# Optimization experiments

Measured on AMD Instinct MI355X. Metric: run time of the kernel, lower is better.

## Reference

```python
import jax, jax.numpy as jnp
import numpy as np

L = 96
K = 3  # conv kernel size

def setup_inputs() -> dict:
    key = jax.random.key(0)
    ks = jax.random.split(key, 6)
    linear_x = jax.random.randint(ks[0], (4 * L**3,), 0, 2, dtype=jnp.int32)
    tetraeder_2 = jax.random.normal(ks[1], (2, 2), dtype=jnp.float32)
    w1 = jax.random.normal(ks[2], (K, K, K, 12, 16), dtype=jnp.float32) * 0.05
    b1 = jnp.zeros((16,), dtype=jnp.float32)
    w2 = jax.random.normal(ks[3], (K, K, K, 16, 32), dtype=jnp.float32) * 0.05
    b2 = jnp.zeros((32,), dtype=jnp.float32)
    wd = jax.random.normal(ks[4], (32, 1), dtype=jnp.float32) * 0.1
    return {"linear_x": linear_x, "tetraeder_2": tetraeder_2,
            "w1": w1, "b1": b1, "w2": w2, "b2": b2, "wd": wd}

def _bonds(linear_x, tetraeder_2):
    # x: (L,L,L,4) spin config; v: (L,L,L,4,d) per-site vectors via gather
    x = linear_x.reshape(L, L, L, 4)
    v = tetraeder_2[x]
    v0, v1, v2, v3 = v[..., 0, :], v[..., 1, :], v[..., 2, :], v[..., 3, :]
    # roll(v, 1, ax)[a] == v[(a-1) % L] -> periodic neighbor cells cell_1/2/3
    r1 = jnp.roll(v1, 1, axis=0)
    r2 = jnp.roll(v2, 1, axis=1)
    r3 = jnp.roll(v3, 1, axis=2)
    dot = lambda a, b: jnp.einsum('...d,...d->...', a, b)
    # 12 bonds in the exact order of on_unit_cell
    bonds = [dot(v0, v1), dot(v0, v2), dot(v0, v3),
             dot(v0, r1), dot(v0, r2), dot(v0, r3),
             dot(v1, v2), dot(v2, v3), dot(v3, v1),
             dot(r1, r2), dot(r2, r3), dot(r3, r1)]
    return jnp.stack(bonds, axis=-1)  # (L,L,L,12)

def _conv_block(y, w, b):
    pad = [(0, 0)] + [((K - 1) // 2, K // 2)] * 3 + [(0, 0)]
    y = jnp.pad(y, pad, mode='wrap')
    y = jax.lax.conv_general_dilated(
        y, w, window_strides=(1, 1, 1), padding='VALID',
        dimension_numbers=('NDHWC', 'DHWIO', 'NDHWC'))
    return jax.nn.elu(y + b)

def reference(linear_x, tetraeder_2, w1, b1, w2, b2, wd):
    y = _bonds(linear_x, tetraeder_2)[jnp.newaxis, ...]  # (1,L,L,L,12)
    y = _conv_block(y, w1, b1)
    y = _conv_block(y, w2, b2)
    y = jnp.mean(y, axis=(1, 2, 3)).ravel()  # (32,)
    return (y @ wd).ravel()[0]
```

## Files before the change

### kernel.cpp

```cpp
#include <hip/hip_runtime.h>
#include <hip/hip_bf16.h>
#include <cmath>

#define L 96
#define L3 (L*L*L)
#define NT 4
#define NCONV 864
#define BSTRIDE 456

__device__ __constant__ const int TAU[27] = {
    0,16,32, 288,304,320, 576,592,608,
    1728,1744,1760, 2016,2032,2048, 2304,2320,2336,
    3456,3472,3488, 3744,3760,3776, 4032,4048,4064};

typedef __attribute__((ext_vector_type(8))) short short8;
typedef __attribute__((ext_vector_type(4))) float floatx4;

__device__ __forceinline__ float eluf(float x) {
    float e = __expf(x) - 1.0f;
    return x > 0.0f ? x : e;
}

__device__ __forceinline__ unsigned short f2bf(float f) {
    __hip_bfloat16 h = __float2bfloat16(f);
    return *reinterpret_cast<unsigned short*>(&h);
}

__device__ __forceinline__ int wrapc(int x) {
    if (x < 0) x += L;
    if (x >= L) x -= L;
    return x;
}

__global__ __launch_bounds__(256) void prep_kernel(
    const int* __restrict__ lx, const float* __restrict__ tet,
    const float* __restrict__ w1, const float* __restrict__ w2,
    unsigned short* __restrict__ bnd,
    unsigned short* __restrict__ Bm1, unsigned short* __restrict__ Bm2)
{
    int idx = blockIdx.x * 256 + threadIdx.x;

    if (idx < 16*BSTRIDE) {
        int o = idx / BSTRIDE, k = idx % BSTRIDE;
        int tau = k >> 4, i = k & 15;
        float v = (k < 448 && tau < 27 && i < 12) ? w1[tau*192 + i*16 + o] : 0.0f;
        Bm1[idx] = f2bf(v);
    }
    int j = idx - 16*BSTRIDE;
    if (j >= 0 && j < 32*BSTRIDE) {
        int o = j / BSTRIDE, k = j % BSTRIDE;
        int tau = k >> 4;
        int i = k & 15;
        float v = (k < 448 && tau < 27) ? w2[tau*512 + i*32 + o] : 0.0f;
        Bm2[j] = f2bf(v);
    }

    int w = idx % L;
    int t = idx / L;
    int h = t % L;
    int d = t / L;

    float t00 = tet[0], t01 = tet[1], t10 = tet[2], t11 = tet[3];
    float d00 = t00*t00 + t01*t01;
    float d01 = t00*t10 + t01*t11;
    float d11 = t10*t10 + t11*t11;

    const int4 sv = *reinterpret_cast<const int4*>(lx + 4*idx);
    int s0 = sv.x, s1 = sv.y, s2 = sv.z, s3 = sv.w;
    int dm = (d == 0) ? L-1 : d-1;
    int hm = (h == 0) ? L-1 : h-1;
    int wm = (w == 0) ? L-1 : w-1;
    int r1 = lx[4*((dm*L + h)*L + w) + 1];
    int r2 = lx[4*((d*L + hm)*L + w) + 2];
    int r3 = lx[4*((d*L + h)*L + wm) + 3];

    auto dot = [&](int a, int b) -> float {
        return (a == b) ? (a ? d11 : d00) : d01;
    };

    union { unsigned short s[16]; int4 q[2]; } u;
    u.s[0]  = f2bf(dot(s0, s1));
    u.s[1]  = f2bf(dot(s0, s2));
    u.s[2]  = f2bf(dot(s0, s3));
    u.s[3]  = f2bf(dot(s0, r1));
    u.s[4]  = f2bf(dot(s0, r2));
    u.s[5]  = f2bf(dot(s0, r3));
    u.s[6]  = f2bf(dot(s1, s2));
    u.s[7]  = f2bf(dot(s2, s3));
    u.s[8]  = f2bf(dot(s3, s1));
    u.s[9]  = f2bf(dot(r1, r2));
    u.s[10] = f2bf(dot(r2, r3));
    u.s[11] = f2bf(dot(r3, r1));
    u.s[12] = 0; u.s[13] = 0; u.s[14] = 0; u.s[15] = 0;

    int4* dst = reinterpret_cast<int4*>(bnd + (size_t)idx*16);
    dst[0] = u.q[0];
    dst[1] = u.q[1];
}

__device__ __forceinline__ void stage_tile(
    const unsigned short* __restrict__ x, unsigned short* __restrict__ tile,
    int W0, int H0, int D0, int tid)
{
    #pragma unroll
    for (int i = 0; i < 6; ++i) {
        int t = tid + i*256;
        if (i < 5 || t < 1296) {
            int row = t / 36, off = t - row*36;
            int dd = row / 6, hh = row - dd*6;
            int gd = wrapc(D0 + dd - 1);
            int gh = wrapc(H0 + hh - 1);
            int vox = off >> 1, half = off & 1;
            int gw = wrapc(W0 + vox - 1);
            size_t gi = ((size_t)((gd*L + gh)*L + gw))*16 + half*8;
            __builtin_amdgcn_global_load_lds(
                (const __attribute__((address_space(1))) unsigned int*)(x + gi),
                (__attribute__((address_space(3))) unsigned int*)(tile + t*8),
                16, 0, 0);
        }
    }
}

__device__ __forceinline__ void stage_bmat(
    const unsigned short* __restrict__ Bm, unsigned short* __restrict__ Bls,
    int nxfer, int tid)
{
    #pragma unroll
    for (int i = 0; i < 8; ++i) {
        int t = tid + i*256;
        if (t < nxfer) {
            __builtin_amdgcn_global_load_lds(
                (const __attribute__((address_space(1))) unsigned int*)(Bm + t*8),
                (__attribute__((address_space(3))) unsigned int*)(Bls + t*8),
                16, 0, 0);
        }
    }
}

__device__ __forceinline__ void tile_coords(int& bid, int& W0, int& H0, int& Dz)
{
    bid = (blockIdx.z * 24 + blockIdx.y) * 6 + blockIdx.x;
    int nb = (bid & 7) * 108 + (bid >> 3);
    W0 = (nb % 6) * 16;
    int t1 = nb / 6;
    H0 = (t1 % 24) * 4;
    Dz = t1 / 24;
}

__global__ __launch_bounds__(256, 2) void conv1_kernel(
    const unsigned short* __restrict__ x, const unsigned short* __restrict__ Bm,
    const float* __restrict__ bias, unsigned short* __restrict__ y)
{
    __shared__ __attribute__((aligned(16))) unsigned short tile[2][6*6*18*16];
    __shared__ __attribute__((aligned(16))) unsigned short Bls[16*BSTRIDE];
    int tid = threadIdx.x;
    int bid, W0, H0, Dz;
    tile_coords(bid, W0, H0, Dz);

    stage_bmat(Bm, Bls, 912, tid);
    stage_tile(x, tile[0], W0, H0, Dz*16, tid);
    __syncthreads();

    int lane = tid & 63, wave = tid >> 6;
    int laneV = lane & 15, g = lane >> 4;
    int gb = g >> 1;
    int abase = laneV*16 + (g & 1)*8;
    float bch = bias[laneV];

    int moff[4];
    #pragma unroll
    for (int m = 0; m < 4; ++m) {
        int mt = wave*4 + m;
        moff[m] = (((mt >> 2)*6 + (mt & 3))*18)*16;
    }

    for (int t = 0; t < NT; ++t) {
        if (t < NT-1)
            stage_tile(x, tile[(t+1) & 1], W0, H0, Dz*16 + 4*(t+1), tid);

        const unsigned short* tl = tile[t & 1];

        floatx4 acc[4];
        #pragma unroll
        for (int m = 0; m < 4; ++m) acc[m] = (floatx4)(0.0f);

        short8 aC[4], aN[4], bC, bN;
        {
            int a0 = abase + (gb ? TAU[1] : TAU[0]);
            bC = *reinterpret_cast<const short8*>(&Bls[laneV*BSTRIDE + g*8]);
            #pragma unroll
            for (int m = 0; m < 4; ++m)
                aC[m] = *reinterpret_cast<const short8*>(&tl[moff[m] + a0]);
        }

        #pragma unroll
        for (int kt = 0; kt < 14; ++kt) {
            if (kt < 13) {
                int tev = TAU[2*(kt+1)];
                int tod = TAU[(2*(kt+1)+1 > 26) ? 26 : 2*(kt+1)+1];
                int an = abase + (gb ? tod : tev);
                bN = *reinterpret_cast<const short8*>(&Bls[laneV*BSTRIDE + (kt+1)*32 + g*8]);
                #pragma unroll
                for (int m = 0; m < 4; ++m)
                    aN[m] = *reinterpret_cast<const short8*>(&tl[moff[m] + an]);
            }
            __builtin_amdgcn_s_setprio(1);
            #pragma unroll
            for (int m = 0; m < 4; ++m)
                acc[m] = __builtin_amdgcn_mfma_f32_16x16x32_bf16(aC[m], bC, acc[m], 0, 0, 0);
            __builtin_amdgcn_s_setprio(0);
            if (kt < 13) {
                #pragma unroll
                for (int m = 0; m < 4; ++m) aC[m] = aN[m];
                bC = bN;
            }
        }

        int D0 = Dz*16 + t*4;
        #pragma unroll
        for (int m = 0; m < 4; ++m) {
            int mt = wave*4 + m;
            int d = D0 + (mt >> 2), h = H0 + (mt & 3);
            int wb = W0 + g*4;
            size_t base = ((size_t)((d*L + h)*L + wb))*16 + laneV;
            #pragma unroll
            for (int reg = 0; reg < 4; ++reg) {
                y[base + (size_t)reg*16] = f2bf(eluf(acc[m][reg] + bch));
            }
        }
        __syncthreads();
    }
}

__global__ __launch_bounds__(256, 2) void conv2_kernel(
    const unsigned short* __restrict__ x, const unsigned short* __restrict__ Bm,
    const float* __restrict__ bias, const float* __restrict__ wd,
    float* __restrict__ partials)
{
    __shared__ __attribute__((aligned(16))) unsigned short tile[2][6*6*18*16];
    __shared__ __attribute__((aligned(16))) unsigned short Bls[32*BSTRIDE];
    __shared__ float red[4];
    int tid = threadIdx.x;
    int bid, W0, H0, Dz;
    tile_coords(bid, W0, H0, Dz);

    stage_bmat(Bm, Bls, 1824, tid);
    stage_tile(x, tile[0], W0, H0, Dz*16, tid);
    __syncthreads();

    int lane = tid & 63, wave = tid >> 6;
    int laneV = lane & 15, g = lane >> 4;
    int gb = g >> 1;
    int abase = laneV*16 + (g & 1)*8;
    float b2a = bias[laneV], b2b = bias[16 + laneV];
    float wda = wd[laneV],  wdb = wd[16 + laneV];

    int moff[4];
    #pragma unroll
    for (int m = 0; m < 4; ++m) {
        int mt = wave*4 + m;
        moff[m] = (((mt >> 2)*6 + (mt & 3))*18)*16;
    }

    float s = 0.0f;

    for (int t = 0; t < NT; ++t) {
        if (t < NT-1)
            stage_tile(x, tile[(t+1) & 1], W0, H0, Dz*16 + 4*(t+1), tid);

        const unsigned short* tl = tile[t & 1];

        floatx4 acc[4][2];
        #pragma unroll
        for (int m = 0; m < 4; ++m) {
            acc[m][0] = (floatx4)(0.0f);
            acc[m][1] = (floatx4)(0.0f);
        }

        short8 aC[4], aN[4], bC0, bC1, bN0, bN1;
        {
            int a0 = abase + (gb ? TAU[1] : TAU[0]);
            bC0 = *reinterpret_cast<const short8*>(&Bls[laneV*BSTRIDE + g*8]);
            bC1 = *reinterpret_cast<const short8*>(&Bls[(16 + laneV)*BSTRIDE + g*8]);
            #pragma unroll
            for (int m = 0; m < 4; ++m)
                aC[m] = *reinterpret_cast<const short8*>(&tl[moff[m] + a0]);
        }

        #pragma unroll
        for (int kt = 0; kt < 14; ++kt) {
            if (kt < 13) {
                int tev = TAU[2*(kt+1)];
                int tod = TAU[(2*(kt+1)+1 > 26) ? 26 : 2*(kt+1)+1];
                int an = abase + (gb ? tod : tev);
                bN0 = *reinterpret_cast<const short8*>(&Bls[laneV*BSTRIDE + (kt+1)*32 + g*8]);
                bN1 = *reinterpret_cast<const short8*>(&Bls[(16 + laneV)*BSTRIDE + (kt+1)*32 + g*8]);
                #pragma unroll
                for (int m = 0; m < 4; ++m)
                    aN[m] = *reinterpret_cast<const short8*>(&tl[moff[m] + an]);
            }
            __builtin_amdgcn_s_setprio(1);
            #pragma unroll
            for (int m = 0; m < 4; ++m) {
                acc[m][0] = __builtin_amdgcn_mfma_f32_16x16x32_bf16(aC[m], bC0, acc[m][0], 0, 0, 0);
                acc[m][1] = __builtin_amdgcn_mfma_f32_16x16x32_bf16(aC[m], bC1, acc[m][1], 0, 0, 0);
            }
            __builtin_amdgcn_s_setprio(0);
            if (kt < 13) {
                #pragma unroll
                for (int m = 0; m < 4; ++m) aC[m] = aN[m];
                bC0 = bN0; bC1 = bN1;
            }
        }

        #pragma unroll
        for (int m = 0; m < 4; ++m) {
            #pragma unroll
            for (int reg = 0; reg < 4; ++reg) {
                s += eluf(acc[m][0][reg] + b2a) * wda;
                s += eluf(acc[m][1][reg] + b2b) * wdb;
            }
        }
        __syncthreads();
    }

    #pragma unroll
    for (int off = 32; off; off >>= 1) s += __shfl_down(s, off);
    if (lane == 0) red[wave] = s;
    __syncthreads();
    if (tid == 0) {
        partials[bid] = red[0] + red[1] + red[2] + red[3];
    }
}

__global__ __launch_bounds__(256) void final_kernel(
    const float* __restrict__ partials, float* __restrict__ out)
{
    float s = 0.0f;
    for (int i = threadIdx.x; i < NCONV; i += 256) s += partials[i];
    #pragma unroll
    for (int off = 32; off; off >>= 1) s += __shfl_down(s, off);
    __shared__ float red[4];
    int lane = threadIdx.x & 63;
    int wv   = threadIdx.x >> 6;
    if (lane == 0) red[wv] = s;
    __syncthreads();
    if (threadIdx.x == 0)
        out[0] = (red[0] + red[1] + red[2] + red[3]) * (1.0f / (float)L3);
}

extern "C" void kernel_launch(void* const* d_in, const int* in_sizes, int n_in,
                              void* d_out, int out_size, void* d_ws, size_t ws_size,
                              hipStream_t stream) {
    const int*   lx  = (const int*)  d_in[0];
    const float* tet = (const float*)d_in[1];
    const float* w1  = (const float*)d_in[2];
    const float* b1  = (const float*)d_in[3];
    const float* w2  = (const float*)d_in[4];
    const float* b2  = (const float*)d_in[5];
    const float* wd  = (const float*)d_in[6];
    float* out = (float*)d_out;

    char* ws = (char*)d_ws;
    const size_t ARR_BYTES = (size_t)L3 * 16 * 2;
    unsigned short* bnd  = (unsigned short*)ws;
    unsigned short* y1   = (unsigned short*)(ws + ARR_BYTES);
    unsigned short* Bm1  = (unsigned short*)(ws + 2*ARR_BYTES);
    unsigned short* Bm2  = (unsigned short*)(ws + 2*ARR_BYTES + 16*BSTRIDE*2);
    float* partials      = (float*)         (ws + 2*ARR_BYTES + 48*BSTRIDE*2);

    prep_kernel<<<L3/256, 256, 0, stream>>>(lx, tet, w1, w2, bnd, Bm1, Bm2);
    conv1_kernel<<<dim3(6,24,6), 256, 0, stream>>>(bnd, Bm1, b1, y1);
    conv2_kernel<<<dim3(6,24,6), 256, 0, stream>>>(y1, Bm2, b2, wd, partials);
    final_kernel<<<1, 256, 0, stream>>>(partials, out);
}
```

Baseline: 151.1 us.

## Fuse bond computation into conv1 halo staging and vectorize output stores

The separate pass that computed the 12 bond features into a global intermediate array is removed. conv1 now loads the spin configuration for its halo tile and neighbour cells, computes the bonds in registers, and writes them into LDS. The global load is issued before the MFMA loop and the LDS write comes after it, so the load latency is overlapped with compute. The MFMA operands are swapped so each lane holds four consecutive output channels, which lets the ELU output be written as one 8-byte store. This avoids writing and re-reading a 56 MB intermediate, at the cost of redundant halo bond computation, scattered 4-byte neighbour loads, and extra register pressure.

```diff
diff --git a/kernel.cpp b/kernel.cpp
--- a/kernel.cpp
+++ b/kernel.cpp
@@ -32,14 +32,11 @@
     return x;
 }
 
-__global__ __launch_bounds__(256) void prep_kernel(
-    const int* __restrict__ lx, const float* __restrict__ tet,
+__global__ __launch_bounds__(256) void prepw_kernel(
     const float* __restrict__ w1, const float* __restrict__ w2,
-    unsigned short* __restrict__ bnd,
     unsigned short* __restrict__ Bm1, unsigned short* __restrict__ Bm2)
 {
     int idx = blockIdx.x * 256 + threadIdx.x;
-
     if (idx < 16*BSTRIDE) {
         int o = idx / BSTRIDE, k = idx % BSTRIDE;
         int tau = k >> 4, i = k & 15;
@@ -54,48 +51,65 @@
         float v = (k < 448 && tau < 27) ? w2[tau*512 + i*32 + o] : 0.0f;
         Bm2[j] = f2bf(v);
     }
-
-    int w = idx % L;
-    int t = idx / L;
-    int h = t % L;
-    int d = t / L;
-
-    float t00 = tet[0], t01 = tet[1], t10 = tet[2], t11 = tet[3];
-    float d00 = t00*t00 + t01*t01;
-    float d01 = t00*t10 + t01*t11;
-    float d11 = t10*t10 + t11*t11;
-
-    const int4 sv = *reinterpret_cast<const int4*>(lx + 4*idx);
-    int s0 = sv.x, s1 = sv.y, s2 = sv.z, s3 = sv.w;
-    int dm = (d == 0) ? L-1 : d-1;
-    int hm = (h == 0) ? L-1 : h-1;
-    int wm = (w == 0) ? L-1 : w-1;
-    int r1 = lx[4*((dm*L + h)*L + w) + 1];
-    int r2 = lx[4*((d*L + hm)*L + w) + 2];
-    int r3 = lx[4*((d*L + h)*L + wm) + 3];
-
-    auto dot = [&](int a, int b) -> float {
-        return (a == b) ? (a ? d11 : d00) : d01;
-    };
-
-    union { unsigned short s[16]; int4 q[2]; } u;
-    u.s[0]  = f2bf(dot(s0, s1));
-    u.s[1]  = f2bf(dot(s0, s2));
-    u.s[2]  = f2bf(dot(s0, s3));
-    u.s[3]  = f2bf(dot(s0, r1));
-    u.s[4]  = f2bf(dot(s0, r2));
-    u.s[5]  = f2bf(dot(s0, r3));
-    u.s[6]  = f2bf(dot(s1, s2));
-    u.s[7]  = f2bf(dot(s2, s3));
-    u.s[8]  = f2bf(dot(s3, s1));
-    u.s[9]  = f2bf(dot(r1, r2));
-    u.s[10] = f2bf(dot(r2, r3));
-    u.s[11] = f2bf(dot(r3, r1));
-    u.s[12] = 0; u.s[13] = 0; u.s[14] = 0; u.s[15] = 0;
-
-    int4* dst = reinterpret_cast<int4*>(bnd + (size_t)idx*16);
-    dst[0] = u.q[0];
-    dst[1] = u.q[1];
+}
+
+__device__ __forceinline__ void bonds_load(
+    const int* __restrict__ lx, int W0, int H0, int D0, int tid,
+    int4* sv, int* n1, int* n2, int* n3)
+{
+    #pragma unroll
+    for (int i = 0; i < 3; ++i) {
+        int t = tid + i*256;
+        if (t < 648) {
+            int dd = t / 108, rem = t - dd*108;
+            int hh = rem / 18, ww = rem - hh*18;
+            int gd = wrapc(D0 + dd - 1);
+            int gh = wrapc(H0 + hh - 1);
+            int gw = wrapc(W0 + ww - 1);
+            int gdm = (gd == 0) ? L-1 : gd-1;
+            int ghm = (gh == 0) ? L-1 : gh-1;
+            int gwm = (gw == 0) ? L-1 : gw-1;
+            sv[i] = *reinterpret_cast<const int4*>(lx + 4*((gd*L + gh)*L + gw));
+            n1[i] = lx[4*((gdm*L + gh)*L + gw) + 1];
+            n2[i] = lx[4*((gd*L + ghm)*L + gw) + 2];
+            n3[i] = lx[4*((gd*L + gh)*L + gwm) + 3];
+        }
+    }
+}
+
+__device__ __forceinline__ void bonds_write(
+    unsigned short* __restrict__ tile, int tid,
+    float d00, float d01, float d11,
+    const int4* sv, const int* n1, const int* n2, const int* n3)
+{
+    #pragma unroll
+    for (int i = 0; i < 3; ++i) {
+        int t = tid + i*256;
+        if (t < 648) {
+            int s0 = sv[i].x, s1 = sv[i].y, s2 = sv[i].z, s3 = sv[i].w;
+            int r1 = n1[i], r2 = n2[i], r3 = n3[i];
+            auto dot = [&](int a, int b) -> float {
+                return (a == b) ? (a ? d11 : d00) : d01;
+            };
+            union { unsigned short s[16]; int4 q[2]; } u;
+            u.s[0]  = f2bf(dot(s0, s1));
+            u.s[1]  = f2bf(dot(s0, s2));
+            u.s[2]  = f2bf(dot(s0, s3));
+            u.s[3]  = f2bf(dot(s0, r1));
+            u.s[4]  = f2bf(dot(s0, r2));
+            u.s[5]  = f2bf(dot(s0, r3));
+            u.s[6]  = f2bf(dot(s1, s2));
+            u.s[7]  = f2bf(dot(s2, s3));
+            u.s[8]  = f2bf(dot(s3, s1));
+            u.s[9]  = f2bf(dot(r1, r2));
+            u.s[10] = f2bf(dot(r2, r3));
+            u.s[11] = f2bf(dot(r3, r1));
+            u.s[12] = 0; u.s[13] = 0; u.s[14] = 0; u.s[15] = 0;
+            int4* dst = reinterpret_cast<int4*>(tile + t*16);
+            dst[0] = u.q[0];
+            dst[1] = u.q[1];
+        }
+    }
 }
 
 __device__ __forceinline__ void stage_tile(
@@ -148,7 +162,8 @@
 }
 
 __global__ __launch_bounds__(256, 2) void conv1_kernel(
-    const unsigned short* __restrict__ x, const unsigned short* __restrict__ Bm,
+    const int* __restrict__ lx, const float* __restrict__ tet,
+    const unsigned short* __restrict__ Bm,
     const float* __restrict__ bias, unsigned short* __restrict__ y)
 {
     __shared__ __attribute__((aligned(16))) unsigned short tile[2][6*6*18*16];
@@ -157,15 +172,26 @@
     int bid, W0, H0, Dz;
     tile_coords(bid, W0, H0, Dz);
 
+    float t00 = tet[0], t01 = tet[1], t10 = tet[2], t11 = tet[3];
+    float d00 = t00*t00 + t01*t01;
+    float d01 = t00*t10 + t01*t11;
+    float d11 = t10*t10 + t11*t11;
+
     stage_bmat(Bm, Bls, 912, tid);
-    stage_tile(x, tile[0], W0, H0, Dz*16, tid);
+
+    int4 sv[3]; int n1[3], n2[3], n3[3];
+    bonds_load(lx, W0, H0, Dz*16, tid, sv, n1, n2, n3);
+    bonds_write(tile[0], tid, d00, d01, d11, sv, n1, n2, n3);
     __syncthreads();
 
     int lane = tid & 63, wave = tid >> 6;
     int laneV = lane & 15, g = lane >> 4;
     int gb = g >> 1;
     int abase = laneV*16 + (g & 1)*8;
-    float bch = bias[laneV];
+
+    float bch[4];
+    #pragma unroll
+    for (int r = 0; r < 4; ++r) bch[r] = bias[g*4 + r];
 
     int moff[4];
     #pragma unroll
@@ -176,7 +202,7 @@
 
     for (int t = 0; t < NT; ++t) {
         if (t < NT-1)
-            stage_tile(x, tile[(t+1) & 1], W0, H0, Dz*16 + 4*(t+1), tid);
+            bonds_load(lx, W0, H0, Dz*16 + 4*(t+1), tid, sv, n1, n2, n3);
 
         const unsigned short* tl = tile[t & 1];
 
@@ -207,7 +233,7 @@
             __builtin_amdgcn_s_setprio(1);
             #pragma unroll
             for (int m = 0; m < 4; ++m)
-                acc[m] = __builtin_amdgcn_mfma_f32_16x16x32_bf16(aC[m], bC, acc[m], 0, 0, 0);
+                acc[m] = __builtin_amdgcn_mfma_f32_16x16x32_bf16(bC, aC[m], acc[m], 0, 0, 0);
             __builtin_amdgcn_s_setprio(0);
             if (kt < 13) {
                 #pragma unroll
@@ -216,17 +242,20 @@
             }
         }
 
+        if (t < NT-1)
+            bonds_write(tile[(t+1) & 1], tid, d00, d01, d11, sv, n1, n2, n3);
+
         int D0 = Dz*16 + t*4;
         #pragma unroll
         for (int m = 0; m < 4; ++m) {
             int mt = wave*4 + m;
             int d = D0 + (mt >> 2), h = H0 + (mt & 3);
-            int wb = W0 + g*4;
-            size_t base = ((size_t)((d*L + h)*L + wb))*16 + laneV;
-            #pragma unroll
-            for (int reg = 0; reg < 4; ++reg) {
-                y[base + (size_t)reg*16] = f2bf(eluf(acc[m][reg] + bch));
-            }
+            int w = W0 + laneV;
+            union { unsigned short s[4]; uint2 v; } o;
+            #pragma unroll
+            for (int r = 0; r < 4; ++r)
+                o.s[r] = f2bf(eluf(acc[m][r] + bch[r]));
+            *reinterpret_cast<uint2*>(&y[((size_t)((d*L + h)*L + w))*16 + g*4]) = o.v;
         }
         __syncthreads();
     }
@@ -363,14 +392,13 @@
 
     char* ws = (char*)d_ws;
     const size_t ARR_BYTES = (size_t)L3 * 16 * 2;
-    unsigned short* bnd  = (unsigned short*)ws;
-    unsigned short* y1   = (unsigned short*)(ws + ARR_BYTES);
-    unsigned short* Bm1  = (unsigned short*)(ws + 2*ARR_BYTES);
-    unsigned short* Bm2  = (unsigned short*)(ws + 2*ARR_BYTES + 16*BSTRIDE*2);
-    float* partials      = (float*)         (ws + 2*ARR_BYTES + 48*BSTRIDE*2);
-
-    prep_kernel<<<L3/256, 256, 0, stream>>>(lx, tet, w1, w2, bnd, Bm1, Bm2);
-    conv1_kernel<<<dim3(6,24,6), 256, 0, stream>>>(bnd, Bm1, b1, y1);
+    unsigned short* y1   = (unsigned short*)ws;
+    unsigned short* Bm1  = (unsigned short*)(ws + ARR_BYTES);
+    unsigned short* Bm2  = (unsigned short*)(ws + ARR_BYTES + 16*BSTRIDE*2);
+    float* partials      = (float*)         (ws + ARR_BYTES + 48*BSTRIDE*2);
+
+    prepw_kernel<<<86, 256, 0, stream>>>(w1, w2, Bm1, Bm2);
+    conv1_kernel<<<dim3(6,24,6), 256, 0, stream>>>(lx, tet, Bm1, b1, y1);
     conv2_kernel<<<dim3(6,24,6), 256, 0, stream>>>(y1, Bm2, b2, wd, partials);
     final_kernel<<<1, 256, 0, stream>>>(partials, out);
 }
```

Result: slower. 160.1 us (+5.9%).
